# Kernel tuning notes

Measured on AMD Instinct MI355X. Metric: run time of the kernel, lower is better.

## Reference

```python
import jax, jax.numpy as jnp
import numpy as np
from jax import lax

H = 512  # hidden_size

def run_layer(x_seq, m_seq, wih, bih, whh, reverse):
    """One directional highway-LSTM layer.
    x_seq: [T,B,in], m_seq: [T,B,1], wih: [6H,in], bih: [6H], whh: [5H,H].
    Returns (out [T,B,H], (h_T, c_T))."""
    T, B, _ = x_seq.shape
    # input projection for all timesteps at once: [T,B,6H]
    xproj = jnp.einsum('tbi,gi->tbg', x_seq, wih) + bih
    h0 = jnp.zeros((B, H), dtype=x_seq.dtype)
    c0 = jnp.zeros((B, H), dtype=x_seq.dtype)

    def step(carry, inp):
        h, c = carry
        xp, m = inp  # xp: [B,6H], m: [B,1]
        preact = h @ whh.T + xp[:, :5 * H]
        i, f, o, t, j = jnp.split(preact, 5, axis=1)
        i = jax.nn.sigmoid(i)
        f = jax.nn.sigmoid(f + 1.0)
        o = jax.nn.sigmoid(o)
        t = jax.nn.sigmoid(t)
        j = jnp.tanh(j)
        k = xp[:, 5 * H:]
        c_new = f * c + i * j
        c_new = m * c_new + (1.0 - m) * c
        h_new = t * o * jnp.tanh(c_new) + (1.0 - t) * k
        h_new = m * h_new + (1.0 - m) * h
        return (h_new, c_new), h_new

    (hT, cT), outs = lax.scan(step, (h0, c0), (xproj, m_seq), reverse=reverse)
    return outs, (hT, cT)


def setup_inputs() -> dict:
    key = jax.random.key(0)
    ks = jax.random.split(key, 16)
    T, B, IN = 512, 32, 512
    s_ih = 1.0 / np.sqrt(IN)
    s_hh = 1.0 / np.sqrt(H)
    d = {
        'x': jax.random.normal(ks[0], (T, B, IN), jnp.float32),
        'masks': jnp.ones((T, B, 1), jnp.float32),
    }
    i = 1
    for tag in ['f0', 'b0', 'f1', 'b1']:
        d['wih_' + tag] = jax.random.normal(ks[i], (6 * H, IN), jnp.float32) * s_ih; i += 1
        d['bih_' + tag] = jnp.zeros((6 * H,), jnp.float32)
        d['whh_' + tag] = jax.random.normal(ks[i], (5 * H, H), jnp.float32) * s_hh; i += 1
    return d


def reference(x, masks, wih_f0, bih_f0, whh_f0, wih_b0, bih_b0, whh_b0,
              wih_f1, bih_f1, whh_f1, wih_b1, bih_b1, whh_b1):
    # layer 0 forward then backward (backward consumes forward's output)
    out_f0, (hf0, cf0) = run_layer(x, masks, wih_f0, bih_f0, whh_f0, reverse=False)
    out_b0, (hb0, cb0) = run_layer(out_f0, masks, wih_b0, bih_b0, whh_b0, reverse=True)
    # layer 1: input is the backward output of layer 0
    out_f1, (hf1, cf1) = run_layer(out_b0, masks, wih_f1, bih_f1, whh_f1, reverse=False)
    out_b1, (hb1, cb1) = run_layer(out_f1, masks, wih_b1, bih_b1, whh_b1, reverse=True)
    h_n = jnp.stack([hf0, hb0, hf1, hb1], axis=0)  # [4,B,H]
    c_n = jnp.stack([cf0, cb0, cf1, cb1], axis=0)
    return out_b1, h_n, c_n
```

## Files before the change

kernel.cpp:

```cpp
#include <hip/hip_runtime.h>
#include <hip/hip_bf16.h>
#include <stdint.h>
#include <stddef.h>
#include <math.h>

#define HH 512
#define TT 512
#define BB 32
#define XH 3072
#define GH 2560
#define NWG 32
#define UPW 16
#define NGRP 2
#define RPG 16
#define KCH 16
#define HSK 520
#define SCOPE __HIP_MEMORY_SCOPE_AGENT
#define WGSC  __HIP_MEMORY_SCOPE_WORKGROUP

typedef __attribute__((ext_vector_type(8))) short bf16x8;
typedef __attribute__((ext_vector_type(4))) float f32x4;
typedef unsigned long long u64;

__device__ __forceinline__ float bf2f(unsigned short u){
  union{float f; unsigned int i;} v; v.i = ((unsigned int)u)<<16; return v.f;
}
__device__ __forceinline__ unsigned short f2bf(float f){
  union{float f; unsigned int i;} v; v.f=f;
  unsigned int x=v.i;
  return (unsigned short)((x + 0x7FFFu + ((x>>16)&1u))>>16);
}
__device__ __forceinline__ float sigm(float x){ return 1.f/(1.f+__expf(-x)); }
__device__ __forceinline__ float tanh_f(float x){ return 1.f - 2.f/(__expf(2.f*x)+1.f); }

__global__ void fill_sentinel_f(float* out, int n, float v){
  int i = blockIdx.x*blockDim.x + threadIdx.x;
  int stride = gridDim.x*blockDim.x;
  for (; i < n; i += stride) out[i] = v;
}

__global__ void conv_f2bf(const float* __restrict__ in, unsigned short* __restrict__ out, int n){
  int i = (blockIdx.x*blockDim.x + threadIdx.x)*4;
  int stride = gridDim.x*blockDim.x*4;
  for (; i < n; i += stride){
    float4 v = *(const float4*)(in + i);
    ushort4 o; o.x=f2bf(v.x); o.y=f2bf(v.y); o.z=f2bf(v.z); o.w=f2bf(v.w);
    *(ushort4*)(out + i) = o;
  }
}

#define BM 128
#define BN 128
#define BKK 32

__global__ __launch_bounds__(256)
void gemm_bt(const unsigned short* __restrict__ A, const unsigned short* __restrict__ Bt,
             const float* __restrict__ bias, unsigned short* __restrict__ C,
             int M, int N, int K)
{
  __shared__ unsigned short Alds[BM*BKK];
  __shared__ unsigned short Blds[BN*BKK];
  const int tid = threadIdx.x;
  const int lane = tid & 63;
  const int w = tid >> 6;
  const int gm = blockIdx.y, gn = blockIdx.x;
  const int wm = (w>>1)*64, wn = (w&1)*64;
  const int l15 = lane & 15, l4 = lane >> 4;
  f32x4 acc[4][4] = {};
  for (int k0 = 0; k0 < K; k0 += BKK){
    __syncthreads();
    #pragma unroll
    for (int it = 0; it < 2; ++it){
      int id2 = it*256 + tid;
      int row = id2 >> 2, kc = (id2 & 3)*8;
      *(bf16x8*)&Alds[row*BKK + kc] = *(const bf16x8*)(A + (size_t)(gm*BM+row)*K + k0 + kc);
      *(bf16x8*)&Blds[row*BKK + kc] = *(const bf16x8*)(Bt + (size_t)(gn*BN+row)*K + k0 + kc);
    }
    __syncthreads();
    bf16x8 af[4], bfv[4];
    #pragma unroll
    for (int i=0;i<4;i++) af[i]  = *(const bf16x8*)&Alds[(wm + i*16 + l15)*BKK + l4*8];
    #pragma unroll
    for (int j=0;j<4;j++) bfv[j] = *(const bf16x8*)&Blds[(wn + j*16 + l15)*BKK + l4*8];
    #pragma unroll
    for (int i=0;i<4;i++)
      #pragma unroll
      for (int j=0;j<4;j++)
        acc[i][j] = __builtin_amdgcn_mfma_f32_16x16x32_bf16(af[i], bfv[j], acc[i][j], 0,0,0);
  }
  #pragma unroll
  for (int i=0;i<4;i++){
    int row0 = gm*BM + wm + i*16 + l4*4;
    #pragma unroll
    for (int j=0;j<4;j++){
      int col = gn*BN + wn + j*16 + l15;
      float bz = bias[col];
      #pragma unroll
      for (int r=0;r<4;r++)
        C[(size_t)(row0+r)*N + col] = f2bf(acc[i][j][r] + bz);
    }
  }
}

__global__ __launch_bounds__(512)
void lstm_scan_v8(const unsigned short* __restrict__ xp,
                  const float* __restrict__ whh,
                  const float* __restrict__ masks,
                  unsigned short* __restrict__ abf,
                  float* __restrict__ outF,
                  float* __restrict__ hT_out, float* __restrict__ cT_out,
                  int* __restrict__ flags,
                  int reverse)
{
  __shared__ __align__(16) unsigned short hs[KCH*HSK];
  __shared__ float pre[5][RPG][17];
  __shared__ unsigned short xps[2][6][RPG][16];
  __shared__ float mlds[2][RPG];
  __shared__ __align__(8) unsigned short pwl[RPG*16];
  __shared__ int go_l;

  const int gid = blockIdx.x & 1;
  const int wgi = blockIdx.x >> 1;
  const int tid = threadIdx.x, wv = tid >> 6, lane = tid & 63;
  const int l15 = lane & 15, l4 = lane >> 4;
  const int u0 = wgi*UPW;
  const int r0 = gid*RPG;
  int* gflags = flags + gid*NWG*16;
  int* myflag = gflags + wgi*16;

  if (tid == 0) go_l = 0;

  bf16x8 Bhi[KCH], Blo[KCH];
  if (wv < 5){
    const float* wrow = whh + ((size_t)(wv*HH + u0 + l15))*HH + l4*8;
    #pragma unroll
    for (int kc = 0; kc < KCH; ++kc){
      float4 v0 = *(const float4*)(wrow + kc*32);
      float4 v1 = *(const float4*)(wrow + kc*32 + 4);
      float vv[8] = {v0.x,v0.y,v0.z,v0.w,v1.x,v1.y,v1.z,v1.w};
      bf16x8 hh, ll;
      #pragma unroll
      for (int j = 0; j < 8; ++j){
        unsigned short hb = f2bf(vv[j]);
        hh[j] = (short)hb;
        ll[j] = (short)f2bf(vv[j] - bf2f(hb));
      }
      Bhi[kc] = hh; Blo[kc] = ll;
    }
  }

  if (wv == 6){
    const int t0 = reverse ? (TT-1) : 0;
    #pragma unroll
    for (int it = 0; it < 3; ++it){
      int p = it*64 + lane;
      int half = p & 1, pg = p >> 1;
      int g = pg % 6, row = pg / 6;
      *(uint4*)&xps[0][g][row][half*8] =
        *(const uint4*)(xp + ((size_t)t0*BB + r0 + row)*XH + g*HH + u0 + half*8);
    }
    if (lane < RPG) mlds[0][lane] = masks[t0*BB + r0 + lane];
  }

  const int r4 = lane >> 4, uu = lane & 15;
  float c_st[4] = {0,0,0,0}, h_st[4] = {0,0,0,0};

  for (int s = 0; s < TT; ++s){
    const int t = reverse ? (TT-1-s) : s;
    if (s > 0){
      if (wv == 7){
        for (;;){
          int v = (lane < NWG)
            ? __hip_atomic_load(gflags + lane*16, __ATOMIC_RELAXED, SCOPE) : s;
          if (__all(v >= s)) break;
          __builtin_amdgcn_s_sleep(1);
        }
        if (lane == 0) __hip_atomic_store(&go_l, s, __ATOMIC_RELAXED, WGSC);
      } else {
        while (__hip_atomic_load(&go_l, __ATOMIC_RELAXED, WGSC) < s)
          __builtin_amdgcn_s_sleep(1);
      }
      const int tp = reverse ? (t+1) : (t-1);
      const u64* src = (const u64*)(abf + ((size_t)tp*BB + r0)*HH);
      #pragma unroll
      for (int it = 0; it < 4; ++it){
        int j = it*512 + tid;
        u64 v = __hip_atomic_load(&src[j], __ATOMIC_RELAXED, SCOPE);
        int r = j >> 7, ww = j & 127;
        int kc = ww >> 3, q4 = (ww >> 1) & 3, half = ww & 1;
        *(u64*)&hs[kc*HSK + (q4*16 + r)*8 + half*4] = v;
      }
    }
    __syncthreads();
    if (s > 0 && wv < 5){
      f32x4 a1 = {0.f,0.f,0.f,0.f}, a2 = {0.f,0.f,0.f,0.f};
      #pragma unroll
      for (int kc = 0; kc < KCH; ++kc){
        bf16x8 A = *(const bf16x8*)&hs[kc*HSK + lane*8];
        a1 = __builtin_amdgcn_mfma_f32_16x16x32_bf16(A, Bhi[kc], a1, 0,0,0);
        a2 = __builtin_amdgcn_mfma_f32_16x16x32_bf16(A, Blo[kc], a2, 0,0,0);
      }
      #pragma unroll
      for (int r = 0; r < 4; ++r) pre[wv][l4*4 + r][l15] = a1[r] + a2[r];
    }
    if (wv == 6 && s+1 < TT){
      const int t1 = reverse ? (t-1) : (t+1);
      const int nb = (s+1) & 1;
      #pragma unroll
      for (int it = 0; it < 3; ++it){
        int p = it*64 + lane;
        int half = p & 1, pg = p >> 1;
        int g = pg % 6, row = pg / 6;
        *(uint4*)&xps[nb][g][row][half*8] =
          *(const uint4*)(xp + ((size_t)t1*BB + r0 + row)*XH + g*HH + u0 + half*8);
      }
      if (lane < RPG) mlds[nb][lane] = masks[t1*BB + r0 + lane];
    }
    __syncthreads();
    if (wv == 5){
      const int sb = s & 1;
      float hvals[4];
      #pragma unroll
      for (int i = 0; i < 4; ++i){
        const int row = r4 + i*4;
        float p0=0,p1=0,p2=0,p3=0,p4=0;
        if (s > 0){
          p0 = pre[0][row][uu]; p1 = pre[1][row][uu]; p2 = pre[2][row][uu];
          p3 = pre[3][row][uu]; p4 = pre[4][row][uu];
        }
        float xi = bf2f(xps[sb][0][row][uu]);
        float xf = bf2f(xps[sb][1][row][uu]);
        float xo = bf2f(xps[sb][2][row][uu]);
        float xg = bf2f(xps[sb][3][row][uu]);
        float xj = bf2f(xps[sb][4][row][uu]);
        float xk = bf2f(xps[sb][5][row][uu]);
        float mm = mlds[sb][row];
        float ig = sigm(p0 + xi);
        float fg = sigm(p1 + xf + 1.0f);
        float og = sigm(p2 + xo);
        float tg = sigm(p3 + xg);
        float jg = tanh_f(p4 + xj);
        float cn = fg*c_st[i] + ig*jg;
        cn = mm*cn + (1.f-mm)*c_st[i];
        float hn = tg*og*tanh_f(cn) + (1.f-tg)*xk;
        hn = mm*hn + (1.f-mm)*h_st[i];
        c_st[i] = cn; h_st[i] = hn;
        hvals[i] = hn;
        pwl[row*16 + uu] = f2bf(hn);
      }
      __threadfence_block();
      {
        int row = lane >> 2, q = lane & 3;
        u64 v = *(const u64*)&pwl[row*16 + q*4];
        u64* dstp = (u64*)(abf + ((size_t)t*BB + r0 + row)*HH + u0 + q*4);
        __hip_atomic_store(dstp, v, __ATOMIC_RELAXED, SCOPE);
      }
      asm volatile("s_waitcnt vmcnt(0)" ::: "memory");
      if (lane == 0)
        __hip_atomic_store(myflag, s+1, __ATOMIC_RELAXED, SCOPE);
      if (outF){
        #pragma unroll
        for (int i = 0; i < 4; ++i)
          outF[((size_t)t*BB + r0 + r4 + i*4)*HH + u0 + uu] = hvals[i];
      }
    }
  }
  if (wv == 5){
    #pragma unroll
    for (int i = 0; i < 4; ++i){
      int row = r0 + r4 + i*4;
      hT_out[(size_t)row*HH + u0 + uu] = h_st[i];
      cT_out[(size_t)row*HH + u0 + uu] = c_st[i];
    }
  }
}

extern "C" void kernel_launch(void* const* d_in, const int* in_sizes, int n_in,
                              void* d_out, int out_size, void* d_ws, size_t ws_size,
                              hipStream_t stream)
{
  const float* x = nullptr; const float* masks = nullptr;
  const float* wih[4] = {}; const float* bih[4] = {}; const float* whh[4] = {};
  int nw = 0, nb = 0, nh = 0;
  for (int i = 0; i < n_in; ++i){
    const int sz = in_sizes[i];
    const float* p = (const float*)d_in[i];
    if      (sz == TT*BB*HH){ if (!x) x = p; }
    else if (sz == TT*BB)   { if (!masks) masks = p; }
    else if (sz == XH*HH)   { if (nw < 4) wih[nw++] = p; }
    else if (sz == XH)      { if (nb < 4) bih[nb++] = p; }
    else if (sz == GH*HH)   { if (nh < 4) whh[nh++] = p; }
  }
  float* out = (float*)d_out;
  if (!x || !masks || nw != 4 || nb != 4 || nh != 4){
    fill_sentinel_f<<<512, 256, 0, stream>>>(out, out_size, 777.0f);
    return;
  }

  char* ws = (char*)d_ws;
  size_t off = 0;
  auto alloc = [&](size_t bytes)->void*{
    void* p = ws + off; off += (bytes + 255) & ~(size_t)255; return p;
  };
  unsigned short* xbf   = (unsigned short*)alloc((size_t)TT*BB*HH*2);
  unsigned short* abf   = (unsigned short*)alloc((size_t)TT*BB*HH*2);
  unsigned short* wbf   = (unsigned short*)alloc((size_t)XH*HH*2);
  unsigned short* xproj = (unsigned short*)alloc((size_t)TT*BB*XH*2);
  int*            flags = (int*)alloc((size_t)4*NGRP*NWG*16*4);

  (void)hipMemsetAsync(flags, 0, (size_t)4*NGRP*NWG*16*4, stream);

  const int thr = 256;
  auto cgrid = [&](int n){ int g = (n/4 + thr - 1)/thr; return g > 2048 ? 2048 : g; };
  conv_f2bf<<<cgrid(TT*BB*HH), thr, 0, stream>>>(x, xbf, TT*BB*HH);

  float* hn = out + (size_t)TT*BB*HH;
  float* cn = hn + (size_t)4*BB*HH;

  for (int L = 0; L < 4; ++L){
    const int rev = L & 1;
    conv_f2bf<<<cgrid(XH*HH), thr, 0, stream>>>(wih[L], wbf, XH*HH);
    gemm_bt<<<dim3(XH/BN, (TT*BB)/BM), 256, 0, stream>>>(
        (L == 0 ? xbf : abf), wbf, bih[L], xproj, TT*BB, XH, HH);

    lstm_scan_v8<<<NGRP*NWG, 512, 0, stream>>>(
        xproj, whh[L], masks, abf,
        (L == 3) ? out : nullptr,
        hn + (size_t)L*BB*HH, cn + (size_t)L*BB*HH,
        flags + (size_t)L*NGRP*NWG*16,
        rev);
  }
}
```

Measured before the change: 8.979 ms.

## Replace per-step flag barrier with poison-sentinel polling on hidden-state data

Result: faster. 8.587 ms (-4.4%).

```diff
diff --git a/kernel.cpp b/kernel.cpp
--- a/kernel.cpp
+++ b/kernel.cpp
@@ -15,8 +15,8 @@
 #define RPG 16
 #define KCH 16
 #define HSK 520
+#define POISON64 0xFFFFFFFFFFFFFFFFULL
 #define SCOPE __HIP_MEMORY_SCOPE_AGENT
-#define WGSC  __HIP_MEMORY_SCOPE_WORKGROUP
 
 typedef __attribute__((ext_vector_type(8))) short bf16x8;
 typedef __attribute__((ext_vector_type(4))) float f32x4;
@@ -103,13 +103,12 @@
 }
 
 __global__ __launch_bounds__(512)
-void lstm_scan_v8(const unsigned short* __restrict__ xp,
+void lstm_scan_v9(const unsigned short* __restrict__ xp,
                   const float* __restrict__ whh,
                   const float* __restrict__ masks,
-                  unsigned short* __restrict__ abf,
+                  unsigned short* __restrict__ ab,
                   float* __restrict__ outF,
                   float* __restrict__ hT_out, float* __restrict__ cT_out,
-                  int* __restrict__ flags,
                   int reverse)
 {
   __shared__ __align__(16) unsigned short hs[KCH*HSK];
@@ -117,7 +116,6 @@
   __shared__ unsigned short xps[2][6][RPG][16];
   __shared__ float mlds[2][RPG];
   __shared__ __align__(8) unsigned short pwl[RPG*16];
-  __shared__ int go_l;
 
   const int gid = blockIdx.x & 1;
   const int wgi = blockIdx.x >> 1;
@@ -125,10 +123,6 @@
   const int l15 = lane & 15, l4 = lane >> 4;
   const int u0 = wgi*UPW;
   const int r0 = gid*RPG;
-  int* gflags = flags + gid*NWG*16;
-  int* myflag = gflags + wgi*16;
-
-  if (tid == 0) go_l = 0;
 
   bf16x8 Bhi[KCH], Blo[KCH];
   if (wv < 5){
@@ -168,27 +162,30 @@
   for (int s = 0; s < TT; ++s){
     const int t = reverse ? (TT-1-s) : s;
     if (s > 0){
-      if (wv == 7){
-        for (;;){
-          int v = (lane < NWG)
-            ? __hip_atomic_load(gflags + lane*16, __ATOMIC_RELAXED, SCOPE) : s;
-          if (__all(v >= s)) break;
-          __builtin_amdgcn_s_sleep(1);
+      const int tp = reverse ? (t+1) : (t-1);
+      const u64* src = (const u64*)(ab + ((size_t)tp*BB + r0)*HH);
+      u64 v[4];
+      #pragma unroll
+      for (int it = 0; it < 4; ++it)
+        v[it] = __hip_atomic_load(&src[it*512 + tid], __ATOMIC_RELAXED, SCOPE);
+      for (;;){
+        bool bad = false;
+        #pragma unroll
+        for (int it = 0; it < 4; ++it){
+          if (v[it] == POISON64){
+            v[it] = __hip_atomic_load(&src[it*512 + tid], __ATOMIC_RELAXED, SCOPE);
+            bad = true;
+          }
         }
-        if (lane == 0) __hip_atomic_store(&go_l, s, __ATOMIC_RELAXED, WGSC);
-      } else {
-        while (__hip_atomic_load(&go_l, __ATOMIC_RELAXED, WGSC) < s)
-          __builtin_amdgcn_s_sleep(1);
-      }
-      const int tp = reverse ? (t+1) : (t-1);
-      const u64* src = (const u64*)(abf + ((size_t)tp*BB + r0)*HH);
+        if (!bad) break;
+        __builtin_amdgcn_s_sleep(1);
+      }
       #pragma unroll
       for (int it = 0; it < 4; ++it){
         int j = it*512 + tid;
-        u64 v = __hip_atomic_load(&src[j], __ATOMIC_RELAXED, SCOPE);
         int r = j >> 7, ww = j & 127;
         int kc = ww >> 3, q4 = (ww >> 1) & 3, half = ww & 1;
-        *(u64*)&hs[kc*HSK + (q4*16 + r)*8 + half*4] = v;
+        *(u64*)&hs[kc*HSK + (q4*16 + r)*8 + half*4] = v[it];
       }
     }
     __syncthreads();
@@ -252,12 +249,9 @@
       {
         int row = lane >> 2, q = lane & 3;
         u64 v = *(const u64*)&pwl[row*16 + q*4];
-        u64* dstp = (u64*)(abf + ((size_t)t*BB + r0 + row)*HH + u0 + q*4);
+        u64* dstp = (u64*)(ab + ((size_t)t*BB + r0 + row)*HH + u0 + q*4);
         __hip_atomic_store(dstp, v, __ATOMIC_RELAXED, SCOPE);
       }
-      asm volatile("s_waitcnt vmcnt(0)" ::: "memory");
-      if (lane == 0)
-        __hip_atomic_store(myflag, s+1, __ATOMIC_RELAXED, SCOPE);
       if (outF){
         #pragma unroll
         for (int i = 0; i < 4; ++i)
@@ -303,12 +297,10 @@
     void* p = ws + off; off += (bytes + 255) & ~(size_t)255; return p;
   };
   unsigned short* xbf   = (unsigned short*)alloc((size_t)TT*BB*HH*2);
-  unsigned short* abf   = (unsigned short*)alloc((size_t)TT*BB*HH*2);
+  unsigned short* ab0   = (unsigned short*)alloc((size_t)TT*BB*HH*2);
+  unsigned short* ab1   = (unsigned short*)alloc((size_t)TT*BB*HH*2);
   unsigned short* wbf   = (unsigned short*)alloc((size_t)XH*HH*2);
   unsigned short* xproj = (unsigned short*)alloc((size_t)TT*BB*XH*2);
-  int*            flags = (int*)alloc((size_t)4*NGRP*NWG*16*4);
-
-  (void)hipMemsetAsync(flags, 0, (size_t)4*NGRP*NWG*16*4, stream);
 
   const int thr = 256;
   auto cgrid = [&](int n){ int g = (n/4 + thr - 1)/thr; return g > 2048 ? 2048 : g; };
@@ -317,17 +309,21 @@
   float* hn = out + (size_t)TT*BB*HH;
   float* cn = hn + (size_t)4*BB*HH;
 
+  unsigned short* ab[2] = {ab0, ab1};
+
   for (int L = 0; L < 4; ++L){
     const int rev = L & 1;
+    unsigned short* cur  = ab[L & 1];
+    const unsigned short* prev = (L == 0) ? xbf : ab[(L+1) & 1];
     conv_f2bf<<<cgrid(XH*HH), thr, 0, stream>>>(wih[L], wbf, XH*HH);
     gemm_bt<<<dim3(XH/BN, (TT*BB)/BM), 256, 0, stream>>>(
-        (L == 0 ? xbf : abf), wbf, bih[L], xproj, TT*BB, XH, HH);
-
-    lstm_scan_v8<<<NGRP*NWG, 512, 0, stream>>>(
-        xproj, whh[L], masks, abf,
+        prev, wbf, bih[L], xproj, TT*BB, XH, HH);
+    (void)hipMemsetAsync(cur, 0xFF, (size_t)TT*BB*HH*2, stream);
+
+    lstm_scan_v9<<<NGRP*NWG, 512, 0, stream>>>(
+        xproj, whh[L], masks, cur,
         (L == 3) ? out : nullptr,
         hn + (size_t)L*BB*HH, cn + (size_t)L*BB*HH,
-        flags + (size_t)L*NGRP*NWG*16,
         rev);
   }
 }
```
